# Kernel optimization log

Hardware: AMD Instinct MI355X
Metric: run time of the kernel (lower is better)

The kernel has to match this reference:

```python
import jax, jax.numpy as jnp
import numpy as np

ROBOT_W = 1.0
PHASE_W = 1.0
COHER_W = 10.0
SPEED_W = 5.0
MAX_SPEED = 10.0
SMOOTH_VEL_W = 0.05
SMOOTH_ACC_W = 0.01

# illegal phase transitions {(0,2),(1,0),(2,0),(2,1)} as a 3x3 lookup table
_ILLEGAL = np.zeros((3, 3), dtype=bool)
for a, b in [(0, 2), (1, 0), (2, 0), (2, 1)]:
    _ILLEGAL[a, b] = True
ILLEGAL_TABLE = jnp.asarray(_ILLEGAL)


def setup_inputs() -> dict:
    key = jax.random.key(0)
    k1, k2, k3, k4 = jax.random.split(key, 4)
    B, T = 256, 8192
    # scale by 8 so per-frame speeds (norm of diffs of 3-vectors) exceed MAX_SPEED
    pred_robot = jax.random.normal(k1, (B, T, 12), dtype=jnp.float32) * 8.0
    gt_robot = jax.random.normal(k2, (B, T, 12), dtype=jnp.float32) * 8.0
    pred_phase = jax.random.normal(k3, (B, T, 3), dtype=jnp.float32)
    gt_phase = jax.random.randint(k4, (B, T), 0, 3, dtype=jnp.int32)
    return {"pred_robot": pred_robot, "pred_phase": pred_phase,
            "gt_robot": gt_robot, "gt_phase": gt_phase}


def _coherence_loss(phase_logits):
    # vectorized replacement for the O(B*T) Python double loop
    p = jnp.argmax(phase_logits, axis=-1)            # [B, T]
    pt, pt1 = p[:, :-1], p[:, 1:]                    # [B, T-1]
    illegal = ILLEGAL_TABLE[pt, pt1]                 # [B, T-1] bool
    # logit of the (illegal) predicted phase at t+1
    sel = jnp.take_along_axis(phase_logits[:, 1:], pt1[..., None], axis=-1)[..., 0]
    loss_sum = jnp.sum(jnp.where(illegal, sel * sel, 0.0))
    count = jnp.sum(illegal)
    return jnp.where(count > 0, loss_sum / jnp.maximum(count, 1).astype(sel.dtype), 0.0)


def _speed_loss(pred_robot):
    B, T, D = pred_robot.shape
    vel = pred_robot[:, 1:] - pred_robot[:, :-1]     # [B, T-1, 12]
    pts = vel.reshape(B, T - 1, 4, 3)
    speeds = jnp.linalg.norm(pts, axis=-1)           # [B, T-1, 4]
    pen = jax.nn.relu(speeds - MAX_SPEED)
    return SPEED_W * jnp.mean(pen * pen)


def reference(pred_robot, pred_phase, gt_robot, gt_phase):
    # MSE over robot trajectory
    robot_loss = jnp.mean((pred_robot - gt_robot) ** 2)
    # cross-entropy over 3 phase classes
    logp = jax.nn.log_softmax(pred_phase, axis=-1)   # [B, T, 3]
    nll = -jnp.take_along_axis(logp, gt_phase[..., None].astype(jnp.int32), axis=-1)[..., 0]
    phase_loss = jnp.mean(nll)
    coherence = _coherence_loss(pred_phase)
    speed_loss = _speed_loss(pred_robot)
    vel = pred_robot[:, 1:] - pred_robot[:, :-1]
    vel_loss = jnp.mean(vel * vel)
    acc = pred_robot[:, 2:] - 2.0 * pred_robot[:, 1:-1] + pred_robot[:, :-2]
    acc_loss = jnp.mean(acc * acc)
    total = (ROBOT_W * robot_loss + PHASE_W * phase_loss + COHER_W * coherence
             + speed_loss + SMOOTH_VEL_W * vel_loss + SMOOTH_ACC_W * acc_loss)
    return total
```

## Files before the change

kernel.cpp:

```cpp
#include <hip/hip_runtime.h>
#include <math.h>

#define B_DIM 256
#define T_DIM 8192
#define BLOCK 256
#define CHUNKS_PER_B (T_DIM / BLOCK)


__global__ __launch_bounds__(BLOCK) void combined_loss_main(
    const float* __restrict__ pred_robot,
    const float* __restrict__ pred_phase,
    const float* __restrict__ gt_robot,
    const int*   __restrict__ gt_phase,
    double* __restrict__ ws)
{
    __shared__ float s_robot[12][BLOCK + 2];
    __shared__ float s_phase[3][BLOCK + 1];
    __shared__ float s_red[4][8];

    const int tid   = threadIdx.x;
    const int b     = blockIdx.x >> 5;
    const int chunk = blockIdx.x & 31;
    const int t0    = chunk << 8;
    const int t     = t0 + tid;

    const size_t row = (size_t)b * T_DIM + t;
    const float* pr = pred_robot + row * 12;
    const float* gr = gt_robot   + row * 12;
    const float* pp = pred_phase + row * 3;

    float r[12], g[12];
    {
        float4 v0 = *(const float4*)(pr);
        float4 v1 = *(const float4*)(pr + 4);
        float4 v2 = *(const float4*)(pr + 8);
        r[0]=v0.x; r[1]=v0.y; r[2]=v0.z; r[3]=v0.w;
        r[4]=v1.x; r[5]=v1.y; r[6]=v1.z; r[7]=v1.w;
        r[8]=v2.x; r[9]=v2.y; r[10]=v2.z; r[11]=v2.w;
        float4 w0 = *(const float4*)(gr);
        float4 w1 = *(const float4*)(gr + 4);
        float4 w2 = *(const float4*)(gr + 8);
        g[0]=w0.x; g[1]=w0.y; g[2]=w0.z; g[3]=w0.w;
        g[4]=w1.x; g[5]=w1.y; g[6]=w1.z; g[7]=w1.w;
        g[8]=w2.x; g[9]=w2.y; g[10]=w2.z; g[11]=w2.w;
    }

    float sse = 0.0f;
    #pragma unroll
    for (int k = 0; k < 12; ++k) { float d = r[k] - g[k]; sse += d * d; }

    #pragma unroll
    for (int k = 0; k < 12; ++k) s_robot[k][tid] = r[k];

    const float l0 = pp[0], l1 = pp[1], l2 = pp[2];
    s_phase[0][tid] = l0; s_phase[1][tid] = l1; s_phase[2][tid] = l2;

    if (tid < 2) {
        const int th = t0 + BLOCK + tid;
        if (th < T_DIM) {
            const float* ph = pred_robot + ((size_t)b * T_DIM + th) * 12;
            #pragma unroll
            for (int k = 0; k < 12; ++k) s_robot[k][BLOCK + tid] = ph[k];
            if (tid == 0) {
                const float* pq = pred_phase + ((size_t)b * T_DIM + th) * 3;
                s_phase[0][BLOCK] = pq[0];
                s_phase[1][BLOCK] = pq[1];
                s_phase[2][BLOCK] = pq[2];
            }
        }
    }

    const int gidx = gt_phase[row];
    float m = fmaxf(l0, fmaxf(l1, l2));
    float lse = m + logf(expf(l0 - m) + expf(l1 - m) + expf(l2 - m));
    float sel = (gidx == 0) ? l0 : ((gidx == 1) ? l1 : l2);
    float nll = lse - sel;

    int p = 0; float pm = l0;
    if (l1 > pm) { pm = l1; p = 1; }
    if (l2 > pm) { pm = l2; p = 2; }

    __syncthreads();

    float csum = 0.0f, ccnt = 0.0f, pen2 = 0.0f, velsq = 0.0f, accsq = 0.0f;

    if (t < T_DIM - 1) {
        float r1[12];
        #pragma unroll
        for (int k = 0; k < 12; ++k) r1[k] = s_robot[k][tid + 1];

        float vel[12];
        #pragma unroll
        for (int k = 0; k < 12; ++k) { vel[k] = r1[k] - r[k]; velsq += vel[k] * vel[k]; }

        #pragma unroll
        for (int j = 0; j < 4; ++j) {
            float sx = vel[3*j], sy = vel[3*j+1], sz = vel[3*j+2];
            float sp = sqrtf(sx*sx + sy*sy + sz*sz);
            float d = sp - 10.0f;
            if (d > 0.0f) pen2 += d * d;
        }

        float n0 = s_phase[0][tid + 1], n1 = s_phase[1][tid + 1], n2 = s_phase[2][tid + 1];
        int p1 = 0; float m1 = n0;
        if (n1 > m1) { m1 = n1; p1 = 1; }
        if (n2 > m1) { m1 = n2; p1 = 2; }
        int mask = (p == 0) ? 4 : ((p == 1) ? 1 : 3);
        if ((mask >> p1) & 1) { csum += m1 * m1; ccnt += 1.0f; }

        if (t < T_DIM - 2) {
            #pragma unroll
            for (int k = 0; k < 12; ++k) {
                float a = s_robot[k][tid + 2] - 2.0f * r1[k] + r[k];
                accsq += a * a;
            }
        }
    }

    float vals[7] = { sse, nll, csum, ccnt, pen2, velsq, accsq };
    #pragma unroll
    for (int off = 32; off > 0; off >>= 1) {
        #pragma unroll
        for (int q = 0; q < 7; ++q)
            vals[q] += __shfl_down(vals[q], off, 64);
    }
    const int wave = tid >> 6, lane = tid & 63;
    if (lane == 0) {
        #pragma unroll
        for (int q = 0; q < 7; ++q) s_red[wave][q] = vals[q];
    }
    __syncthreads();
    if (tid < 7) {
        double acc = (double)s_red[0][tid] + (double)s_red[1][tid]
                   + (double)s_red[2][tid] + (double)s_red[3][tid];
        atomicAdd(&ws[tid], acc);
    }
}

__global__ void combined_loss_final(const double* __restrict__ ws, float* __restrict__ out)
{
    const double robot = ws[0] / (double)((size_t)B_DIM * T_DIM * 12);
    const double phase = ws[1] / (double)((size_t)B_DIM * T_DIM);
    const double coher = (ws[3] > 0.0) ? (ws[2] / fmax(ws[3], 1.0)) : 0.0;
    const double speed = 5.0  * (ws[4] / (double)((size_t)B_DIM * (T_DIM - 1) * 4));
    const double vel   = 0.05 * (ws[5] / (double)((size_t)B_DIM * (T_DIM - 1) * 12));
    const double acc   = 0.01 * (ws[6] / (double)((size_t)B_DIM * (T_DIM - 2) * 12));
    out[0] = (float)(robot + phase + 10.0 * coher + speed + vel + acc);
}

extern "C" void kernel_launch(void* const* d_in, const int* in_sizes, int n_in,
                              void* d_out, int out_size, void* d_ws, size_t ws_size,
                              hipStream_t stream)
{
    const float* pred_robot = (const float*)d_in[0];
    const float* pred_phase = (const float*)d_in[1];
    const float* gt_robot   = (const float*)d_in[2];
    const int*   gt_phase   = (const int*)d_in[3];
    double* ws  = (double*)d_ws;
    float*  out = (float*)d_out;

    hipMemsetAsync(d_ws, 0, 7 * sizeof(double), stream);

    const dim3 grid(B_DIM * CHUNKS_PER_B);
    combined_loss_main<<<grid, BLOCK, 0, stream>>>(pred_robot, pred_phase, gt_robot, gt_phase, ws);
    combined_loss_final<<<1, 1, 0, stream>>>(ws, out);
}
```

Before: 278.7 us.

## Coalesce robot and phase loads via float4 staging and spread atomics across slots

```diff
diff --git a/kernel.cpp b/kernel.cpp
--- a/kernel.cpp
+++ b/kernel.cpp
@@ -5,18 +5,19 @@
 #define T_DIM 8192
 #define BLOCK 256
 #define CHUNKS_PER_B (T_DIM / BLOCK)
+#define NSLOT 256
 
 
 __global__ __launch_bounds__(BLOCK) void combined_loss_main(
-    const float* __restrict__ pred_robot,
-    const float* __restrict__ pred_phase,
-    const float* __restrict__ gt_robot,
-    const int*   __restrict__ gt_phase,
+    const float4* __restrict__ pred4,
+    const float*  __restrict__ pred_phase,
+    const float4* __restrict__ gt4,
+    const int*    __restrict__ gt_phase,
     double* __restrict__ ws)
 {
-    __shared__ float s_robot[12][BLOCK + 2];
-    __shared__ float s_phase[3][BLOCK + 1];
-    __shared__ float s_red[4][8];
+    __shared__ float4 sp[774];
+    __shared__ float  s_ph[776];
+    __shared__ float  s_red[4][8];
 
     const int tid   = threadIdx.x;
     const int b     = blockIdx.x >> 5;
@@ -24,53 +25,43 @@
     const int t0    = chunk << 8;
     const int t     = t0 + tid;
 
-    const size_t row = (size_t)b * T_DIM + t;
-    const float* pr = pred_robot + row * 12;
-    const float* gr = gt_robot   + row * 12;
-    const float* pp = pred_phase + row * 3;
+    const size_t row0  = (size_t)b * T_DIM + t0;
+    const size_t base4 = row0 * 3;
+    const float4* ph4  = (const float4*)pred_phase + ((row0 * 3) >> 2);
+    const bool halo = (t0 + BLOCK) < T_DIM;
 
-    float r[12], g[12];
+    float4 p0 = pred4[base4 + tid];
+    float4 p1 = pred4[base4 + tid + 256];
+    float4 p2 = pred4[base4 + tid + 512];
+    float4 g0 = gt4[base4 + tid];
+    float4 g1 = gt4[base4 + tid + 256];
+    float4 g2 = gt4[base4 + tid + 512];
+    float4 ph = make_float4(0.f, 0.f, 0.f, 0.f);
+    if (tid < 192) ph = ph4[tid];
+    const int gidx = gt_phase[row0 + tid];
+    if (halo && tid >= 248 && tid < 254)
+        sp[768 + (tid - 248)] = pred4[base4 + 768 + (tid - 248)];
+    if (halo && tid >= 192 && tid < 198)
+        s_ph[768 + (tid - 192)] = pred_phase[row0 * 3 + 768 + (tid - 192)];
+
+    float sse = 0.0f;
     {
-        float4 v0 = *(const float4*)(pr);
-        float4 v1 = *(const float4*)(pr + 4);
-        float4 v2 = *(const float4*)(pr + 8);
-        r[0]=v0.x; r[1]=v0.y; r[2]=v0.z; r[3]=v0.w;
-        r[4]=v1.x; r[5]=v1.y; r[6]=v1.z; r[7]=v1.w;
-        r[8]=v2.x; r[9]=v2.y; r[10]=v2.z; r[11]=v2.w;
-        float4 w0 = *(const float4*)(gr);
-        float4 w1 = *(const float4*)(gr + 4);
-        float4 w2 = *(const float4*)(gr + 8);
-        g[0]=w0.x; g[1]=w0.y; g[2]=w0.z; g[3]=w0.w;
-        g[4]=w1.x; g[5]=w1.y; g[6]=w1.z; g[7]=w1.w;
-        g[8]=w2.x; g[9]=w2.y; g[10]=w2.z; g[11]=w2.w;
+        float d;
+        d = p0.x - g0.x; sse += d*d;  d = p0.y - g0.y; sse += d*d;
+        d = p0.z - g0.z; sse += d*d;  d = p0.w - g0.w; sse += d*d;
+        d = p1.x - g1.x; sse += d*d;  d = p1.y - g1.y; sse += d*d;
+        d = p1.z - g1.z; sse += d*d;  d = p1.w - g1.w; sse += d*d;
+        d = p2.x - g2.x; sse += d*d;  d = p2.y - g2.y; sse += d*d;
+        d = p2.z - g2.z; sse += d*d;  d = p2.w - g2.w; sse += d*d;
     }
 
-    float sse = 0.0f;
-    #pragma unroll
-    for (int k = 0; k < 12; ++k) { float d = r[k] - g[k]; sse += d * d; }
+    sp[tid]       = p0;
+    sp[tid + 256] = p1;
+    sp[tid + 512] = p2;
+    if (tid < 192) *((float4*)&s_ph[4 * tid]) = ph;
+    __syncthreads();
 
-    #pragma unroll
-    for (int k = 0; k < 12; ++k) s_robot[k][tid] = r[k];
-
-    const float l0 = pp[0], l1 = pp[1], l2 = pp[2];
-    s_phase[0][tid] = l0; s_phase[1][tid] = l1; s_phase[2][tid] = l2;
-
-    if (tid < 2) {
-        const int th = t0 + BLOCK + tid;
-        if (th < T_DIM) {
-            const float* ph = pred_robot + ((size_t)b * T_DIM + th) * 12;
-            #pragma unroll
-            for (int k = 0; k < 12; ++k) s_robot[k][BLOCK + tid] = ph[k];
-            if (tid == 0) {
-                const float* pq = pred_phase + ((size_t)b * T_DIM + th) * 3;
-                s_phase[0][BLOCK] = pq[0];
-                s_phase[1][BLOCK] = pq[1];
-                s_phase[2][BLOCK] = pq[2];
-            }
-        }
-    }
-
-    const int gidx = gt_phase[row];
+    const float l0 = s_ph[3*tid], l1 = s_ph[3*tid + 1], l2 = s_ph[3*tid + 2];
     float m = fmaxf(l0, fmaxf(l1, l2));
     float lse = m + logf(expf(l0 - m) + expf(l1 - m) + expf(l2 - m));
     float sel = (gidx == 0) ? l0 : ((gidx == 1) ? l1 : l2);
@@ -80,39 +71,41 @@
     if (l1 > pm) { pm = l1; p = 1; }
     if (l2 > pm) { pm = l2; p = 2; }
 
-    __syncthreads();
-
     float csum = 0.0f, ccnt = 0.0f, pen2 = 0.0f, velsq = 0.0f, accsq = 0.0f;
 
+    float4 a0 = sp[tid*3], a1 = sp[tid*3 + 1], a2 = sp[tid*3 + 2];
+    float rA[12] = { a0.x,a0.y,a0.z,a0.w, a1.x,a1.y,a1.z,a1.w, a2.x,a2.y,a2.z,a2.w };
+
     if (t < T_DIM - 1) {
-        float r1[12];
-        #pragma unroll
-        for (int k = 0; k < 12; ++k) r1[k] = s_robot[k][tid + 1];
+        float4 b0 = sp[tid*3 + 3], b1 = sp[tid*3 + 4], b2 = sp[tid*3 + 5];
+        float rB[12] = { b0.x,b0.y,b0.z,b0.w, b1.x,b1.y,b1.z,b1.w, b2.x,b2.y,b2.z,b2.w };
 
         float vel[12];
         #pragma unroll
-        for (int k = 0; k < 12; ++k) { vel[k] = r1[k] - r[k]; velsq += vel[k] * vel[k]; }
+        for (int k = 0; k < 12; ++k) { vel[k] = rB[k] - rA[k]; velsq += vel[k]*vel[k]; }
 
         #pragma unroll
         for (int j = 0; j < 4; ++j) {
             float sx = vel[3*j], sy = vel[3*j+1], sz = vel[3*j+2];
-            float sp = sqrtf(sx*sx + sy*sy + sz*sz);
-            float d = sp - 10.0f;
-            if (d > 0.0f) pen2 += d * d;
+            float sp2 = sqrtf(sx*sx + sy*sy + sz*sz);
+            float d = sp2 - 10.0f;
+            if (d > 0.0f) pen2 += d*d;
         }
 
-        float n0 = s_phase[0][tid + 1], n1 = s_phase[1][tid + 1], n2 = s_phase[2][tid + 1];
-        int p1 = 0; float m1 = n0;
-        if (n1 > m1) { m1 = n1; p1 = 1; }
-        if (n2 > m1) { m1 = n2; p1 = 2; }
+        float n0 = s_ph[3*tid + 3], n1 = s_ph[3*tid + 4], n2 = s_ph[3*tid + 5];
+        int p1i = 0; float m1 = n0;
+        if (n1 > m1) { m1 = n1; p1i = 1; }
+        if (n2 > m1) { m1 = n2; p1i = 2; }
         int mask = (p == 0) ? 4 : ((p == 1) ? 1 : 3);
-        if ((mask >> p1) & 1) { csum += m1 * m1; ccnt += 1.0f; }
+        if ((mask >> p1i) & 1) { csum += m1*m1; ccnt += 1.0f; }
 
         if (t < T_DIM - 2) {
+            float4 c0 = sp[tid*3 + 6], c1 = sp[tid*3 + 7], c2 = sp[tid*3 + 8];
+            float rC[12] = { c0.x,c0.y,c0.z,c0.w, c1.x,c1.y,c1.z,c1.w, c2.x,c2.y,c2.z,c2.w };
             #pragma unroll
             for (int k = 0; k < 12; ++k) {
-                float a = s_robot[k][tid + 2] - 2.0f * r1[k] + r[k];
-                accsq += a * a;
+                float a = rC[k] - 2.0f*rB[k] + rA[k];
+                accsq += a*a;
             }
         }
     }
@@ -133,35 +126,59 @@
     if (tid < 7) {
         double acc = (double)s_red[0][tid] + (double)s_red[1][tid]
                    + (double)s_red[2][tid] + (double)s_red[3][tid];
-        atomicAdd(&ws[tid], acc);
+        atomicAdd(&ws[(size_t)(blockIdx.x & (NSLOT - 1)) * 8 + tid], acc);
     }
 }
 
-__global__ void combined_loss_final(const double* __restrict__ ws, float* __restrict__ out)
+__global__ __launch_bounds__(256) void combined_loss_final(
+    const double* __restrict__ ws, float* __restrict__ out)
 {
-    const double robot = ws[0] / (double)((size_t)B_DIM * T_DIM * 12);
-    const double phase = ws[1] / (double)((size_t)B_DIM * T_DIM);
-    const double coher = (ws[3] > 0.0) ? (ws[2] / fmax(ws[3], 1.0)) : 0.0;
-    const double speed = 5.0  * (ws[4] / (double)((size_t)B_DIM * (T_DIM - 1) * 4));
-    const double vel   = 0.05 * (ws[5] / (double)((size_t)B_DIM * (T_DIM - 1) * 12));
-    const double acc   = 0.01 * (ws[6] / (double)((size_t)B_DIM * (T_DIM - 2) * 12));
-    out[0] = (float)(robot + phase + 10.0 * coher + speed + vel + acc);
+    __shared__ double sred[4][7];
+    const int tid = threadIdx.x;
+    double v[7];
+    #pragma unroll
+    for (int q = 0; q < 7; ++q) v[q] = ws[(size_t)tid * 8 + q];
+    #pragma unroll
+    for (int off = 32; off > 0; off >>= 1) {
+        #pragma unroll
+        for (int q = 0; q < 7; ++q)
+            v[q] += __shfl_down(v[q], off, 64);
+    }
+    const int wave = tid >> 6, lane = tid & 63;
+    if (lane == 0) {
+        #pragma unroll
+        for (int q = 0; q < 7; ++q) sred[wave][q] = v[q];
+    }
+    __syncthreads();
+    if (tid == 0) {
+        double s[7];
+        #pragma unroll
+        for (int q = 0; q < 7; ++q)
+            s[q] = sred[0][q] + sred[1][q] + sred[2][q] + sred[3][q];
+        const double robot = s[0] / (double)((size_t)B_DIM * T_DIM * 12);
+        const double phase = s[1] / (double)((size_t)B_DIM * T_DIM);
+        const double coher = (s[3] > 0.0) ? (s[2] / fmax(s[3], 1.0)) : 0.0;
+        const double speed = 5.0  * (s[4] / (double)((size_t)B_DIM * (T_DIM - 1) * 4));
+        const double vel   = 0.05 * (s[5] / (double)((size_t)B_DIM * (T_DIM - 1) * 12));
+        const double acc   = 0.01 * (s[6] / (double)((size_t)B_DIM * (T_DIM - 2) * 12));
+        out[0] = (float)(robot + phase + 10.0 * coher + speed + vel + acc);
+    }
 }
 
 extern "C" void kernel_launch(void* const* d_in, const int* in_sizes, int n_in,
                               void* d_out, int out_size, void* d_ws, size_t ws_size,
                               hipStream_t stream)
 {
-    const float* pred_robot = (const float*)d_in[0];
-    const float* pred_phase = (const float*)d_in[1];
-    const float* gt_robot   = (const float*)d_in[2];
-    const int*   gt_phase   = (const int*)d_in[3];
+    const float4* pred4      = (const float4*)d_in[0];
+    const float*  pred_phase = (const float*)d_in[1];
+    const float4* gt4        = (const float4*)d_in[2];
+    const int*    gt_phase   = (const int*)d_in[3];
     double* ws  = (double*)d_ws;
     float*  out = (float*)d_out;
 
-    hipMemsetAsync(d_ws, 0, 7 * sizeof(double), stream);
+    hipMemsetAsync(d_ws, 0, (size_t)NSLOT * 8 * sizeof(double), stream);
 
     const dim3 grid(B_DIM * CHUNKS_PER_B);
-    combined_loss_main<<<grid, BLOCK, 0, stream>>>(pred_robot, pred_phase, gt_robot, gt_phase, ws);
-    combined_loss_final<<<1, 1, 0, stream>>>(ws, out);
+    combined_loss_main<<<grid, BLOCK, 0, stream>>>(pred4, pred_phase, gt4, gt_phase, ws);
+    combined_loss_final<<<1, 256, 0, stream>>>(ws, out);
 }
```

Result: faster. 240.1 us (-13.8%).
